# Performance work log

Measured on AMD Instinct MI355X. Metric: run time of the kernel, lower is better.

Reference implementation:

```python
import jax, jax.numpy as jnp
import numpy as np

HID = 1024
HEADS = 16
HEAD_DIM = HID // HEADS
SCALE = HEAD_DIM ** -0.5


def setup_inputs() -> dict:
    key = jax.random.key(0)
    ks = jax.random.split(key, 11)
    B, S = 4, 2048
    std = HID ** -0.5
    inp = {
        'q': jax.random.normal(ks[0], (B, S, HID), jnp.float32),
        'k': jax.random.normal(ks[1], (B, S, HID), jnp.float32),
        'v': jax.random.normal(ks[2], (B, S, HID), jnp.float32),
        'Wq': jax.random.normal(ks[3], (HID, HID), jnp.float32) * std,
        'bq': jnp.zeros((HID,), jnp.float32),
        'Wk': jax.random.normal(ks[4], (HID, HID), jnp.float32) * std,
        'bk': jnp.zeros((HID,), jnp.float32),
        'Wv': jax.random.normal(ks[5], (HID, HID), jnp.float32) * std,
        'bv': jnp.zeros((HID,), jnp.float32),
        'Wo': jax.random.normal(ks[6], (HID, HID), jnp.float32) * std,
        'bo': jnp.zeros((HID,), jnp.float32),
    }
    return inp


def _split_heads(x, B):
    # [B, S, HID] -> [B, H, S, Dh]
    return x.reshape(B, -1, HEADS, HEAD_DIM).transpose(0, 2, 1, 3)


def reference(q, k, v, Wq, bq, Wk, bk, Wv, bv, Wo, bo):
    B = q.shape[0]
    Q = _split_heads(jnp.dot(q, Wq.T) + bq, B)
    K = _split_heads(jnp.dot(k, Wk.T) + bk, B)
    V = _split_heads(jnp.dot(v, Wv.T) + bv, B)
    # [B, H, Sq, Sk]
    energy = jnp.einsum('bhqd,bhkd->bhqk', Q, K) * SCALE
    attention = jax.nn.softmax(energy, axis=-1)
    x = jnp.einsum('bhqk,bhkd->bhqd', attention, V)  # dropout = identity (eval)
    x = x.transpose(0, 2, 1, 3).reshape(B, -1, HID)
    x = jnp.dot(x, Wo.T) + bo
    return (x, attention)
```

## Files before the change

kernel.cpp:

```cpp
#include <hip/hip_runtime.h>
#include <stdint.h>

#define HID 1024
#define HEADS 16
#define HDIM 64
#define SEQ 2048
#define BATCH 4
#define SCALE 0.125f
#define EXPC 0.18033688011112042f

typedef __bf16 bf16x8 __attribute__((ext_vector_type(8)));
typedef float f32x4 __attribute__((ext_vector_type(4)));
typedef unsigned short ushortx8 __attribute__((ext_vector_type(8)));
typedef unsigned short ushortx4 __attribute__((ext_vector_type(4)));

__device__ __forceinline__ unsigned short f2bf(float f) {
  uint32_t u = __builtin_bit_cast(uint32_t, f);
  u = (u + 0x7fffu + ((u >> 16) & 1u)) >> 16;
  return (unsigned short)u;
}
__device__ __forceinline__ float bf2f(unsigned short u) {
  uint32_t x = ((uint32_t)u) << 16;
  return __builtin_bit_cast(float, x);
}
__device__ __forceinline__ void gl16(const void* g, void* l) {
  __builtin_amdgcn_global_load_lds(
      (const __attribute__((address_space(1))) unsigned int*)g,
      (__attribute__((address_space(3))) unsigned int*)l, 16, 0, 0);
}

struct ConvArgs {
  const float* s[4];
  unsigned short* d[4];
  int n[4];
};
__global__ __launch_bounds__(256) void convk(ConvArgs a) {
  const int ten = blockIdx.y;
  const float* s = a.s[ten];
  unsigned short* d = a.d[ten];
  const int n = a.n[ten];
  const int stride = gridDim.x * blockDim.x * 8;
  for (int i = (blockIdx.x * blockDim.x + threadIdx.x) * 8; i < n; i += stride) {
    float4 v0 = *(const float4*)(s + i);
    float4 v1 = *(const float4*)(s + i + 4);
    ushortx8 o = {f2bf(v0.x), f2bf(v0.y), f2bf(v0.z), f2bf(v0.w),
                  f2bf(v1.x), f2bf(v1.y), f2bf(v1.z), f2bf(v1.w)};
    *(ushortx8*)(d + i) = o;
  }
}

struct QkvArgs {
  const float* Af[3];
  const unsigned short* W[3];
  const float* bias[3];
  unsigned short* out[3];
};
__global__ __launch_bounds__(256) void gemm_qkv(QkvArgs ar) {
  __shared__ unsigned short Als[128 * 64];
  __shared__ unsigned short Bls[128 * 64];
  const int bid = blockIdx.x;
  const int wgid = (bid & 7) * 192 + (bid >> 3);
  const int z = wgid >> 9;
  const int rem = wgid & 511;
  const int bm = rem >> 3, bn = rem & 7;

  const float* Af = ar.Af[z];
  const unsigned short* Wb = ar.W[z];
  const float* bias = ar.bias[z];
  unsigned short* Out = ar.out[z];

  const int t = threadIdx.x;
  const int w = t >> 6, lane = t & 63;
  const int wm = w >> 1, wn = w & 1;
  const int lr = lane & 15, lk = lane >> 4;
  const int row0 = bm * 128, col0 = bn * 128;

  const unsigned short* Wbase =
      Wb + (size_t)(col0 + w * 32 + (lane >> 3)) * HID + (lane & 7) * 8;

  f32x4 acc[4][4] = {};

  for (int ks = 0; ks < 16; ++ks) {
    __syncthreads();
#pragma unroll
    for (int i = 0; i < 4; ++i)
      gl16(Wbase + (size_t)i * 8 * HID + ks * 64, &Bls[(w * 32 + i * 8) * 64]);
#pragma unroll
    for (int i = 0; i < 8; ++i) {
      int chunk = t + i * 256;
      int r = chunk >> 4, c4 = (chunk & 15) * 4;
      float4 v4 = *(const float4*)(Af + (size_t)(row0 + r) * HID + ks * 64 + c4);
      ushortx4 o = {f2bf(v4.x), f2bf(v4.y), f2bf(v4.z), f2bf(v4.w)};
      *(ushortx4*)&Als[r * 64 + c4] = o;
    }
    __syncthreads();
#pragma unroll
    for (int kk = 0; kk < 2; ++kk) {
      bf16x8 a[4], bb[4];
#pragma unroll
      for (int f = 0; f < 4; ++f) {
        a[f] = *(const bf16x8*)&Als[(wm * 64 + f * 16 + lr) * 64 + kk * 32 + lk * 8];
        bb[f] = *(const bf16x8*)&Bls[(wn * 64 + f * 16 + lr) * 64 + kk * 32 + lk * 8];
      }
#pragma unroll
      for (int fm = 0; fm < 4; ++fm)
#pragma unroll
        for (int fn = 0; fn < 4; ++fn)
          acc[fm][fn] = __builtin_amdgcn_mfma_f32_16x16x32_bf16(
              a[fm], bb[fn], acc[fm][fn], 0, 0, 0);
    }
  }

  const float sc = (z == 0) ? EXPC : 1.0f;
#pragma unroll
  for (int fn = 0; fn < 4; ++fn) {
    int col = col0 + wn * 64 + fn * 16 + lr;
    float bv = bias[col];
#pragma unroll
    for (int fm = 0; fm < 4; ++fm) {
      int row = row0 + wm * 64 + fm * 16 + lk * 4;
      if (z == 2) {
        int b_ = row >> 11, s = row & 2047;
        int hh = col >> 6, d = col & 63;
        ushortx4 o4 = {f2bf(acc[fm][fn][0] + bv), f2bf(acc[fm][fn][1] + bv),
                       f2bf(acc[fm][fn][2] + bv), f2bf(acc[fm][fn][3] + bv)};
        *(ushortx4*)(Out + ((size_t)(b_ * HEADS + hh) * HDIM + d) * SEQ + s) = o4;
      } else {
#pragma unroll
        for (int r = 0; r < 4; ++r)
          Out[(size_t)(row + r) * HID + col] = f2bf((acc[fm][fn][r] + bv) * sc);
      }
    }
  }
}

template <int W_F32>
__global__ __launch_bounds__(256) void gemm_wo(
    const unsigned short* __restrict__ A, const void* __restrict__ Wp,
    const float* __restrict__ bias, float* __restrict__ Out) {
  __shared__ unsigned short Als[128 * 64];
  __shared__ unsigned short Bls[128 * 64];
  const int bid = blockIdx.x;
  const int wgid = (bid & 7) * 64 + (bid >> 3);
  const int bm = wgid >> 3, bn = wgid & 7;
  const int t = threadIdx.x;
  const int w = t >> 6, lane = t & 63;
  const int wm = w >> 1, wn = w & 1;
  const int lr = lane & 15, lk = lane >> 4;
  const int row0 = bm * 128, col0 = bn * 128;

  const unsigned short* Abase =
      A + (size_t)(row0 + w * 32 + (lane >> 3)) * HID + (lane & 7) * 8;
  const unsigned short* Wb16 =
      (const unsigned short*)Wp + (size_t)(col0 + w * 32 + (lane >> 3)) * HID +
      (lane & 7) * 8;

  f32x4 acc[4][4] = {};

  for (int ks = 0; ks < 16; ++ks) {
    __syncthreads();
#pragma unroll
    for (int i = 0; i < 4; ++i)
      gl16(Abase + (size_t)i * 8 * HID + ks * 64, &Als[(w * 32 + i * 8) * 64]);
    if (!W_F32) {
#pragma unroll
      for (int i = 0; i < 4; ++i)
        gl16(Wb16 + (size_t)i * 8 * HID + ks * 64, &Bls[(w * 32 + i * 8) * 64]);
    } else {
      const float* Wf = (const float*)Wp;
#pragma unroll
      for (int i = 0; i < 8; ++i) {
        int chunk = t + i * 256;
        int r = chunk >> 4, c4 = (chunk & 15) * 4;
        float4 v4 = *(const float4*)(Wf + (size_t)(col0 + r) * HID + ks * 64 + c4);
        ushortx4 o = {f2bf(v4.x), f2bf(v4.y), f2bf(v4.z), f2bf(v4.w)};
        *(ushortx4*)&Bls[r * 64 + c4] = o;
      }
    }
    __syncthreads();
#pragma unroll
    for (int kk = 0; kk < 2; ++kk) {
      bf16x8 a[4], bb[4];
#pragma unroll
      for (int f = 0; f < 4; ++f) {
        a[f] = *(const bf16x8*)&Als[(wm * 64 + f * 16 + lr) * 64 + kk * 32 + lk * 8];
        bb[f] = *(const bf16x8*)&Bls[(wn * 64 + f * 16 + lr) * 64 + kk * 32 + lk * 8];
      }
#pragma unroll
      for (int fm = 0; fm < 4; ++fm)
#pragma unroll
        for (int fn = 0; fn < 4; ++fn)
          acc[fm][fn] = __builtin_amdgcn_mfma_f32_16x16x32_bf16(
              a[fm], bb[fn], acc[fm][fn], 0, 0, 0);
    }
  }

#pragma unroll
  for (int fn = 0; fn < 4; ++fn) {
    int col = col0 + wn * 64 + fn * 16 + lr;
    float bv = bias[col];
#pragma unroll
    for (int fm = 0; fm < 4; ++fm) {
      int row = row0 + wm * 64 + fm * 16 + lk * 4;
#pragma unroll
      for (int r = 0; r < 4; ++r)
        Out[(size_t)(row + r) * HID + col] = acc[fm][fn][r] + bv;
    }
  }
}

__global__ __launch_bounds__(512) void attn_kern(
    const unsigned short* __restrict__ Qb, const unsigned short* __restrict__ Kb,
    const unsigned short* __restrict__ Vt, float* __restrict__ attn_out,
    unsigned short* __restrict__ Xc) {
  __shared__ unsigned short Qls[128][72];
  __shared__ unsigned short Kls[2][64 * 64];
  __shared__ unsigned short Vls[2][64 * 64];

  const int t = threadIdx.x;
  const int bid = blockIdx.x;
  const int wgid = (bid & 7) * 64 + (bid >> 3);
  const int qbp = wgid & 7;
  const int h = (wgid >> 3) & 15;
  const int b = wgid >> 7;

  const int w = t >> 6, lane = t & 63;
  const int lr = lane & 15, lk = lane >> 4;

  const int srow = lane >> 3;
  const int scol = (lane & 7) ^ srow;
  const unsigned short* gK =
      Kb + ((size_t)b * SEQ + w * 8 + srow) * HID + h * HDIM + scol * 8;
  const unsigned short* gV =
      Vt + ((size_t)(b * HEADS + h) * HDIM + w * 8 + srow) * SEQ + scol * 8;
  unsigned short* lK = &Kls[0][w * 8 * 64];
  unsigned short* lV = &Vls[0][w * 8 * 64];

  for (int qbi = 0; qbi < 2; ++qbi) {
    const int qb = qbp * 2 + qbi;
    const size_t qrow0 = (size_t)b * SEQ + (size_t)qb * 128;

    gl16(gK, lK);
#pragma unroll
    for (int i = 0; i < 2; ++i) {
      int chunk = t + i * 512;
      int r = chunk >> 3, c8 = (chunk & 7) * 8;
      *(ushortx8*)&Qls[r][c8] =
          *(const ushortx8*)(Qb + (qrow0 + r) * HID + h * HDIM + c8);
    }
    __syncthreads();

    bf16x8 qf[2];
#pragma unroll
    for (int kk = 0; kk < 2; ++kk)
      qf[kk] = *(const bf16x8*)&Qls[w * 16 + lr][kk * 32 + lk * 8];
    auto& Pls = Qls;

    float lsum[4] = {0.f, 0.f, 0.f, 0.f};
    int buf = 0;

    for (int kt = 0; kt < 32; ++kt) {
      if (kt < 31) gl16(gK + (size_t)(kt + 1) * 64 * HID, lK + (buf ^ 1) * 4096);
      f32x4 acc[4] = {};
      __builtin_amdgcn_s_setprio(1);
#pragma unroll
      for (int kk = 0; kk < 2; ++kk)
#pragma unroll
        for (int kf = 0; kf < 4; ++kf) {
          bf16x8 bb = *(const bf16x8*)&Kls[buf][(kf * 16 + lr) * 64 +
                                               (((kk * 4 + lk) ^ (lr & 7)) << 3)];
          acc[kf] =
              __builtin_amdgcn_mfma_f32_16x16x32_bf16(qf[kk], bb, acc[kf], 0, 0, 0);
        }
      __builtin_amdgcn_s_setprio(0);
#pragma unroll
      for (int kf = 0; kf < 4; ++kf)
#pragma unroll
        for (int r = 0; r < 4; ++r) lsum[r] += exp2f(acc[kf][r]);
      __syncthreads();
      buf ^= 1;
    }

    float invl[4];
#pragma unroll
    for (int r = 0; r < 4; ++r) {
#pragma unroll
      for (int off = 1; off < 16; off <<= 1) lsum[r] += __shfl_xor(lsum[r], off, 64);
      invl[r] = 1.0f / lsum[r];
    }

    f32x4 oacc[4] = {};
    float* attn_base =
        attn_out + ((size_t)(b * HEADS + h) * SEQ + (size_t)qb * 128) * SEQ;

    gl16(gK, lK);
    gl16(gV, lV);
    __syncthreads();
    for (int kt = 0; kt < 32; ++kt) {
      if (kt < 31) {
        gl16(gK + (size_t)(kt + 1) * 64 * HID, lK + (buf ^ 1) * 4096);
        gl16(gV + (size_t)(kt + 1) * 64, lV + (buf ^ 1) * 4096);
      }
      f32x4 acc[4] = {};
      __builtin_amdgcn_s_setprio(1);
#pragma unroll
      for (int kk = 0; kk < 2; ++kk)
#pragma unroll
        for (int kf = 0; kf < 4; ++kf) {
          bf16x8 bb = *(const bf16x8*)&Kls[buf][(kf * 16 + lr) * 64 +
                                               (((kk * 4 + lk) ^ (lr & 7)) << 3)];
          acc[kf] =
              __builtin_amdgcn_mfma_f32_16x16x32_bf16(qf[kk], bb, acc[kf], 0, 0, 0);
        }
      __builtin_amdgcn_s_setprio(0);
#pragma unroll
      for (int kf = 0; kf < 4; ++kf)
#pragma unroll
        for (int r = 0; r < 4; ++r) {
          float p = exp2f(acc[kf][r]) * invl[r];
          Pls[w * 16 + lk * 4 + r][kf * 16 + lr] = f2bf(p);
        }
#pragma unroll
      for (int it = 0; it < 4; ++it) {
        int rl = it * 4 + lk;
        ushortx4 p4 = *(const ushortx4*)&Pls[w * 16 + rl][lr * 4];
        f32x4 o = {bf2f(p4[0]), bf2f(p4[1]), bf2f(p4[2]), bf2f(p4[3])};
        __builtin_nontemporal_store(
            o, (f32x4*)(attn_base + (size_t)(w * 16 + rl) * SEQ + kt * 64 + lr * 4));
      }
      __builtin_amdgcn_s_setprio(1);
#pragma unroll
      for (int kk = 0; kk < 2; ++kk) {
        bf16x8 ap = *(const bf16x8*)&Pls[w * 16 + lr][kk * 32 + lk * 8];
#pragma unroll
        for (int df = 0; df < 4; ++df) {
          bf16x8 bv = *(const bf16x8*)&Vls[buf][(df * 16 + lr) * 64 +
                                               (((kk * 4 + lk) ^ (lr & 7)) << 3)];
          oacc[df] = __builtin_amdgcn_mfma_f32_16x16x32_bf16(ap, bv, oacc[df], 0, 0, 0);
        }
      }
      __builtin_amdgcn_s_setprio(0);
      __syncthreads();
      buf ^= 1;
    }

#pragma unroll
    for (int df = 0; df < 4; ++df)
#pragma unroll
      for (int r = 0; r < 4; ++r) {
        int row = w * 16 + lk * 4 + r;
        int col = h * HDIM + df * 16 + lr;
        Xc[(qrow0 + row) * HID + col] = f2bf(oacc[df][r]);
      }
  }
}

extern "C" void kernel_launch(void* const* d_in, const int* in_sizes, int n_in,
                              void* d_out, int out_size, void* d_ws, size_t ws_size,
                              hipStream_t stream) {
  const float* q = (const float*)d_in[0];
  const float* k = (const float*)d_in[1];
  const float* v = (const float*)d_in[2];
  const float* Wq = (const float*)d_in[3];
  const float* bq = (const float*)d_in[4];
  const float* Wk = (const float*)d_in[5];
  const float* bk = (const float*)d_in[6];
  const float* Wv = (const float*)d_in[7];
  const float* bv = (const float*)d_in[8];
  const float* Wo = (const float*)d_in[9];
  const float* bo = (const float*)d_in[10];

  char* ws = (char*)d_ws;
  const size_t MAT = (size_t)8192 * 1024 * sizeof(unsigned short);
  unsigned short* Qbuf = (unsigned short*)(ws);
  unsigned short* Kbuf = (unsigned short*)(ws + MAT);
  unsigned short* Vtb = (unsigned short*)(ws + 2 * MAT);
  unsigned short* Xc = (unsigned short*)(ws + 3 * MAT);

  float* xout = (float*)d_out;
  float* attn_out = xout + (size_t)BATCH * SEQ * HID;

  unsigned short* scr = (unsigned short*)attn_out;
  const int NW = 1024 * 1024;
  unsigned short* wq16 = scr;
  unsigned short* wk16 = wq16 + NW;
  unsigned short* wv16 = wk16 + NW;
  unsigned short* wo16 = (unsigned short*)(ws + 4 * MAT);
  const bool wo_bf = ws_size >= 4 * MAT + (size_t)NW * sizeof(unsigned short);

  ConvArgs ca;
  ca.s[0] = Wq; ca.s[1] = Wk; ca.s[2] = Wv; ca.s[3] = Wo;
  ca.d[0] = wq16; ca.d[1] = wk16; ca.d[2] = wv16; ca.d[3] = wo16;
  ca.n[0] = NW; ca.n[1] = NW; ca.n[2] = NW; ca.n[3] = NW;

  dim3 blk(256);
  hipLaunchKernelGGL(convk, dim3(128, wo_bf ? 4 : 3), blk, 0, stream, ca);

  QkvArgs qa;
  qa.Af[0] = q; qa.Af[1] = k; qa.Af[2] = v;
  qa.W[0] = wq16; qa.W[1] = wk16; qa.W[2] = wv16;
  qa.bias[0] = bq; qa.bias[1] = bk; qa.bias[2] = bv;
  qa.out[0] = Qbuf; qa.out[1] = Kbuf; qa.out[2] = Vtb;
  hipLaunchKernelGGL(gemm_qkv, dim3(1536), blk, 0, stream, qa);

  hipLaunchKernelGGL(attn_kern, dim3(512), dim3(512), 0, stream, Qbuf, Kbuf, Vtb,
                     attn_out, Xc);

  if (wo_bf)
    hipLaunchKernelGGL((gemm_wo<0>), dim3(512), blk, 0, stream, Xc, wo16, bo, xout);
  else
    hipLaunchKernelGGL((gemm_wo<1>), dim3(512), blk, 0, stream, Xc, Wo, bo, xout);
}
```

Before: 401.7 us.

## Share K tiles across both query blocks in the softmax-sum pass

The first (row-sum) pass now loads both query blocks' Q fragments up front and streams K once, computing exp-sums for two 128-row blocks per K tile. Previously it streamed K twice. This halves K traffic and barriers in that pass and gives each K fragment load two MFMAs. The cost is more live registers (two accumulator sets), which the added launch-bounds occupancy hint of 4 may pressure or force into spills.

```diff
diff --git a/kernel.cpp b/kernel.cpp
--- a/kernel.cpp
+++ b/kernel.cpp
@@ -209,7 +209,7 @@
   }
 }
 
-__global__ __launch_bounds__(512) void attn_kern(
+__global__ __launch_bounds__(512, 4) void attn_kern(
     const unsigned short* __restrict__ Qb, const unsigned short* __restrict__ Kb,
     const unsigned short* __restrict__ Vt, float* __restrict__ attn_out,
     unsigned short* __restrict__ Xc) {
@@ -236,11 +236,12 @@
   unsigned short* lK = &Kls[0][w * 8 * 64];
   unsigned short* lV = &Vls[0][w * 8 * 64];
 
+  gl16(gK, lK);
+
+  bf16x8 qf[2][2];
+#pragma unroll
   for (int qbi = 0; qbi < 2; ++qbi) {
-    const int qb = qbp * 2 + qbi;
-    const size_t qrow0 = (size_t)b * SEQ + (size_t)qb * 128;
-
-    gl16(gK, lK);
+    const size_t qrow0 = (size_t)b * SEQ + (size_t)(qbp * 2 + qbi) * 128;
 #pragma unroll
     for (int i = 0; i < 2; ++i) {
       int chunk = t + i * 512;
@@ -249,49 +250,59 @@
           *(const ushortx8*)(Qb + (qrow0 + r) * HID + h * HDIM + c8);
     }
     __syncthreads();
-
-    bf16x8 qf[2];
 #pragma unroll
     for (int kk = 0; kk < 2; ++kk)
-      qf[kk] = *(const bf16x8*)&Qls[w * 16 + lr][kk * 32 + lk * 8];
-    auto& Pls = Qls;
-
-    float lsum[4] = {0.f, 0.f, 0.f, 0.f};
-    int buf = 0;
-
-    for (int kt = 0; kt < 32; ++kt) {
-      if (kt < 31) gl16(gK + (size_t)(kt + 1) * 64 * HID, lK + (buf ^ 1) * 4096);
-      f32x4 acc[4] = {};
-      __builtin_amdgcn_s_setprio(1);
-#pragma unroll
-      for (int kk = 0; kk < 2; ++kk)
-#pragma unroll
-        for (int kf = 0; kf < 4; ++kf) {
-          bf16x8 bb = *(const bf16x8*)&Kls[buf][(kf * 16 + lr) * 64 +
-                                               (((kk * 4 + lk) ^ (lr & 7)) << 3)];
-          acc[kf] =
-              __builtin_amdgcn_mfma_f32_16x16x32_bf16(qf[kk], bb, acc[kf], 0, 0, 0);
-        }
-      __builtin_amdgcn_s_setprio(0);
+      qf[qbi][kk] = *(const bf16x8*)&Qls[w * 16 + lr][kk * 32 + lk * 8];
+    __syncthreads();
+  }
+  auto& Pls = Qls;
+
+  float lsum[2][4] = {};
+  int buf = 0;
+  for (int kt = 0; kt < 32; ++kt) {
+    if (kt < 31) gl16(gK + (size_t)(kt + 1) * 64 * HID, lK + (buf ^ 1) * 4096);
+    f32x4 acc[2][4] = {};
+    __builtin_amdgcn_s_setprio(1);
+#pragma unroll
+    for (int kk = 0; kk < 2; ++kk)
+#pragma unroll
+      for (int kf = 0; kf < 4; ++kf) {
+        bf16x8 bb = *(const bf16x8*)&Kls[buf][(kf * 16 + lr) * 64 +
+                                             (((kk * 4 + lk) ^ (lr & 7)) << 3)];
+        acc[0][kf] =
+            __builtin_amdgcn_mfma_f32_16x16x32_bf16(qf[0][kk], bb, acc[0][kf], 0, 0, 0);
+        acc[1][kf] =
+            __builtin_amdgcn_mfma_f32_16x16x32_bf16(qf[1][kk], bb, acc[1][kf], 0, 0, 0);
+      }
+    __builtin_amdgcn_s_setprio(0);
+#pragma unroll
+    for (int qbi = 0; qbi < 2; ++qbi)
 #pragma unroll
       for (int kf = 0; kf < 4; ++kf)
 #pragma unroll
-        for (int r = 0; r < 4; ++r) lsum[r] += exp2f(acc[kf][r]);
-      __syncthreads();
-      buf ^= 1;
-    }
-
-    float invl[4];
+        for (int r = 0; r < 4; ++r) lsum[qbi][r] += exp2f(acc[qbi][kf][r]);
+    __syncthreads();
+    buf ^= 1;
+  }
+
+  float invl[2][4];
+#pragma unroll
+  for (int qbi = 0; qbi < 2; ++qbi)
 #pragma unroll
     for (int r = 0; r < 4; ++r) {
 #pragma unroll
-      for (int off = 1; off < 16; off <<= 1) lsum[r] += __shfl_xor(lsum[r], off, 64);
-      invl[r] = 1.0f / lsum[r];
-    }
-
-    f32x4 oacc[4] = {};
+      for (int off = 1; off < 16; off <<= 1)
+        lsum[qbi][r] += __shfl_xor(lsum[qbi][r], off, 64);
+      invl[qbi][r] = 1.0f / lsum[qbi][r];
+    }
+
+#pragma unroll
+  for (int qbi = 0; qbi < 2; ++qbi) {
+    const int qb = qbp * 2 + qbi;
+    const size_t qrow0 = (size_t)b * SEQ + (size_t)qb * 128;
     float* attn_base =
         attn_out + ((size_t)(b * HEADS + h) * SEQ + (size_t)qb * 128) * SEQ;
+    f32x4 oacc[4] = {};
 
     gl16(gK, lK);
     gl16(gV, lV);
@@ -309,15 +320,15 @@
         for (int kf = 0; kf < 4; ++kf) {
           bf16x8 bb = *(const bf16x8*)&Kls[buf][(kf * 16 + lr) * 64 +
                                                (((kk * 4 + lk) ^ (lr & 7)) << 3)];
-          acc[kf] =
-              __builtin_amdgcn_mfma_f32_16x16x32_bf16(qf[kk], bb, acc[kf], 0, 0, 0);
+          acc[kf] = __builtin_amdgcn_mfma_f32_16x16x32_bf16(qf[qbi][kk], bb, acc[kf],
+                                                            0, 0, 0);
         }
       __builtin_amdgcn_s_setprio(0);
 #pragma unroll
       for (int kf = 0; kf < 4; ++kf)
 #pragma unroll
         for (int r = 0; r < 4; ++r) {
-          float p = exp2f(acc[kf][r]) * invl[r];
+          float p = exp2f(acc[kf][r]) * invl[qbi][r];
           Pls[w * 16 + lk * 4 + r][kf * 16 + lr] = f2bf(p);
         }
 #pragma unroll
@@ -336,7 +347,8 @@
         for (int df = 0; df < 4; ++df) {
           bf16x8 bv = *(const bf16x8*)&Vls[buf][(df * 16 + lr) * 64 +
                                                (((kk * 4 + lk) ^ (lr & 7)) << 3)];
-          oacc[df] = __builtin_amdgcn_mfma_f32_16x16x32_bf16(ap, bv, oacc[df], 0, 0, 0);
+          oacc[df] =
+              __builtin_amdgcn_mfma_f32_16x16x32_bf16(ap, bv, oacc[df], 0, 0, 0);
         }
       }
       __builtin_amdgcn_s_setprio(0);
```

Measured after the change: 403.5 us. About the same (+0.4%).
